# Kernel optimization log

Hardware: AMD Instinct MI355X
Metric: run time of the kernel (lower is better)

## Reference

```python
import jax, jax.numpy as jnp
import numpy as np

N_EMBD = 768
N_HEAD = 8
HEAD_DIM = N_EMBD // N_HEAD
EPS = 1e-5


def _layernorm(x, g, b):
    mu = jnp.mean(x, axis=-1, keepdims=True)
    var = jnp.mean(jnp.square(x - mu), axis=-1, keepdims=True)
    return (x - mu) * jax.lax.rsqrt(var + EPS) * g + b


def _new_gelu(x):
    c = jnp.sqrt(2.0 / jnp.pi).astype(x.dtype)
    return 0.5 * x * (1.0 + jnp.tanh(c * (x + 0.044715 * x * x * x)))


def setup_inputs() -> dict:
    key = jax.random.key(0)
    ks = jax.random.split(key, 10)
    B, T, C = 16, 1024, N_EMBD
    s = lambda fan_in: 1.0 / np.sqrt(fan_in)
    inp = {
        "x": jax.random.normal(ks[0], (B, T, C), dtype=jnp.float32),
        "ln1_g": jnp.ones((C,), jnp.float32),
        "ln1_b": jnp.zeros((C,), jnp.float32),
        "attn_w": jax.random.normal(ks[1], (C, 3 * C), jnp.float32) * s(C),
        "attn_b": jnp.zeros((3 * C,), jnp.float32),
        "proj_w": jax.random.normal(ks[2], (C, C), jnp.float32) * s(C),
        "proj_b": jnp.zeros((C,), jnp.float32),
        "ln2_g": jnp.ones((C,), jnp.float32),
        "ln2_b": jnp.zeros((C,), jnp.float32),
        "fc_w": jax.random.normal(ks[3], (C, 4 * C), jnp.float32) * s(C),
        "fc_b": jnp.zeros((4 * C,), jnp.float32),
        "fc2_w": jax.random.normal(ks[4], (4 * C, C), jnp.float32) * s(4 * C),
        "fc2_b": jnp.zeros((C,), jnp.float32),
    }
    return inp


def reference(x, ln1_g, ln1_b, attn_w, attn_b, proj_w, proj_b,
              ln2_g, ln2_b, fc_w, fc_b, fc2_w, fc2_b):
    B, T, C = x.shape
    H, D = N_HEAD, HEAD_DIM
    scale = 1.0 / np.sqrt(D)

    # --- attention branch ---
    h = _layernorm(x, ln1_g, ln1_b)
    qkv = h @ attn_w + attn_b                       # [B,T,3C]
    q, k, v = jnp.split(qkv, 3, axis=-1)
    q = q.reshape(B, T, H, D).transpose(0, 2, 1, 3)  # [B,H,T,D]
    k = k.reshape(B, T, H, D).transpose(0, 2, 1, 3)
    v = v.reshape(B, T, H, D).transpose(0, 2, 1, 3)
    att = jnp.einsum("bhqd,bhkd->bhqk", q, k) * scale
    causal = jnp.tril(jnp.ones((T, T), bool))
    att = jnp.where(causal, att, -jnp.inf)
    att = jax.nn.softmax(att, axis=-1)
    y = jnp.einsum("bhqk,bhkd->bhqd", att, v)        # [B,H,T,D]
    y = y.transpose(0, 2, 1, 3).reshape(B, T, C)
    y = y @ proj_w + proj_b
    x = x + y

    # --- MLP branch ---
    h2 = _layernorm(x, ln2_g, ln2_b)
    h2 = _new_gelu(h2 @ fc_w + fc_b)
    x = x + (h2 @ fc2_w + fc2_b)
    return x
```

## Files before the change

kernel.cpp:

```cpp
#include <hip/hip_runtime.h>


typedef __bf16 bf16;
typedef __bf16 bf16x8 __attribute__((ext_vector_type(8)));
typedef __bf16 bf16x4 __attribute__((ext_vector_type(4)));
typedef __bf16 bf16x2 __attribute__((ext_vector_type(2)));
typedef float f32x4 __attribute__((ext_vector_type(4)));

__device__ __forceinline__ void async_copy16(const void* g, void* l)
{
    __builtin_amdgcn_global_load_lds((__attribute__((address_space(1))) void*)g,
                                     (__attribute__((address_space(3))) void*)l,
                                     16, 0, 0);
}

__device__ __forceinline__ void bar_nodrain()
{
    __builtin_amdgcn_sched_barrier(0);
    __asm__ volatile("" ::: "memory");
    __builtin_amdgcn_s_barrier();
    __asm__ volatile("" ::: "memory");
    __builtin_amdgcn_sched_barrier(0);
}

__global__ __launch_bounds__(256) void wtrans4(const float* __restrict__ aw, bf16* __restrict__ awT,
                                               const float* __restrict__ pw, bf16* __restrict__ pwT,
                                               const float* __restrict__ fw, bf16* __restrict__ fwT,
                                               const float* __restrict__ f2w, bf16* __restrict__ f2wT)
{
    __shared__ float tile[32][33];
    int id = blockIdx.x;
    const float* in; bf16* out; int R, C, nx;
    if (id < 1728)      { in = aw;  out = awT;  R = 768;  C = 2304; nx = 72; }
    else if (id < 2304) { in = pw;  out = pwT;  R = 768;  C = 768;  nx = 24; id -= 1728; }
    else if (id < 4608) { in = fw;  out = fwT;  R = 768;  C = 3072; nx = 96; id -= 2304; }
    else                { in = f2w; out = f2wT; R = 3072; C = 768;  nx = 24; id -= 4608; }
    const int c0 = (id % nx) * 32, r0 = (id / nx) * 32;
    const int tx = threadIdx.x, ty = threadIdx.y;
#pragma unroll
    for (int i = 0; i < 4; ++i)
        tile[ty + i * 8][tx] = in[(size_t)(r0 + ty + i * 8) * C + c0 + tx];
    __syncthreads();
#pragma unroll
    for (int i = 0; i < 4; ++i)
        out[(size_t)(c0 + ty + i * 8) * R + r0 + tx] = (bf16)tile[tx][ty + i * 8];
}

template <typename TIN>
__global__ __launch_bounds__(256) void ln_kernel(const TIN* __restrict__ x,
                                                 const float* __restrict__ g,
                                                 const float* __restrict__ bb,
                                                 bf16* __restrict__ out)
{
    const int wave = threadIdx.x >> 6, lane = threadIdx.x & 63;
    const size_t row = (size_t)blockIdx.x * 4 + wave;
    const TIN* xr = x + row * 768;
    float v[12];
    float s = 0.f;
    if constexpr (sizeof(TIN) == 2) {
        const bf16x8 t8 = *(const bf16x8*)(xr + lane * 8);
        const bf16x4 t4 = *(const bf16x4*)(xr + 512 + lane * 4);
#pragma unroll
        for (int j = 0; j < 8; ++j) { v[j] = (float)t8[j]; s += v[j]; }
#pragma unroll
        for (int j = 0; j < 4; ++j) { v[8 + j] = (float)t4[j]; s += v[8 + j]; }
    } else {
#pragma unroll
        for (int c = 0; c < 3; ++c) {
            const float4 t4 = *(const float4*)(xr + c * 256 + lane * 4);
            v[c * 4 + 0] = t4.x; v[c * 4 + 1] = t4.y;
            v[c * 4 + 2] = t4.z; v[c * 4 + 3] = t4.w;
            s += t4.x + t4.y + t4.z + t4.w;
        }
    }
#pragma unroll
    for (int off = 32; off >= 1; off >>= 1) s += __shfl_xor(s, off, 64);
    const float mu = s * (1.f / 768.f);
    float q = 0.f;
#pragma unroll
    for (int i = 0; i < 12; ++i) { const float d = v[i] - mu; q += d * d; }
#pragma unroll
    for (int off = 32; off >= 1; off >>= 1) q += __shfl_xor(q, off, 64);
    const float rs = rsqrtf(q * (1.f / 768.f) + 1e-5f);

    if constexpr (sizeof(TIN) == 2) {
        bf16x8 o8; bf16x4 o4;
#pragma unroll
        for (int j = 0; j < 8; ++j) {
            const float gv = g[lane * 8 + j], bv = bb[lane * 8 + j];
            o8[j] = (bf16)((v[j] - mu) * rs * gv + bv);
        }
#pragma unroll
        for (int j = 0; j < 4; ++j) {
            const float gv = g[512 + lane * 4 + j], bv = bb[512 + lane * 4 + j];
            o4[j] = (bf16)((v[8 + j] - mu) * rs * gv + bv);
        }
        *(bf16x8*)(out + row * 768 + lane * 8) = o8;
        *(bf16x4*)(out + row * 768 + 512 + lane * 4) = o4;
    } else {
#pragma unroll
        for (int c = 0; c < 3; ++c) {
            const float4 gv = *(const float4*)(g + c * 256 + lane * 4);
            const float4 bv = *(const float4*)(bb + c * 256 + lane * 4);
            bf16x4 ov;
            ov[0] = (bf16)((v[c * 4 + 0] - mu) * rs * gv.x + bv.x);
            ov[1] = (bf16)((v[c * 4 + 1] - mu) * rs * gv.y + bv.y);
            ov[2] = (bf16)((v[c * 4 + 2] - mu) * rs * gv.z + bv.z);
            ov[3] = (bf16)((v[c * 4 + 3] - mu) * rs * gv.w + bv.w);
            *(bf16x4*)(out + row * 768 + c * 256 + lane * 4) = ov;
        }
    }
}

template <int EPI, int TN>
__global__ __launch_bounds__(256) void gemm_bt(const bf16* __restrict__ A,
                                               const bf16* __restrict__ Bt,
                                               const float* __restrict__ bias,
                                               const void* __restrict__ res,
                                               void* __restrict__ out,
                                               const int M, const int N, const int K)
{
    constexpr int NT_W = TN / 32;
    constexpr int NCPB = (TN * 8) / 256;
    __shared__ bf16 sA[2 * 128 * 32];
    __shared__ bf16 sB[2 * TN * 32];
    const int t = threadIdx.x;
    const int wave = t >> 6, lane = t & 63;
    const int quad = lane >> 4, l16 = lane & 15;
    const int bm0 = blockIdx.x * 128, bn0 = blockIdx.y * TN;
    const int wm = (wave >> 1) * 64, wn = (wave & 1) * (TN / 2);

    const f32x4 z4 = {0.f, 0.f, 0.f, 0.f};
    f32x4 acc[4][NT_W];
#pragma unroll
    for (int i = 0; i < 4; ++i)
#pragma unroll
        for (int j = 0; j < NT_W; ++j) acc[i][j] = z4;

    const bf16* gAp[4]; bf16* lAp[4];
#pragma unroll
    for (int c = 0; c < 4; ++c) {
        const int j = c * 256 + t;
        const int img = j >> 9, r = (j >> 2) & 127, k8 = j & 3;
        gAp[c] = A + (size_t)(bm0 + r) * K + img * 32 + k8 * 8;
        lAp[c] = sA + j * 8;
    }
    const bf16* gBp[NCPB]; bf16* lBp[NCPB];
#pragma unroll
    for (int c = 0; c < NCPB; ++c) {
        const int j = c * 256 + t;
        const int img = j / (TN * 4), r = (j % (TN * 4)) >> 2, k8 = j & 3;
        gBp[c] = Bt + (size_t)(bn0 + r) * K + img * 32 + k8 * 8;
        lBp[c] = sB + j * 8;
    }

    for (int kt = 0; kt < K; kt += 64) {
        __syncthreads();
#pragma unroll
        for (int c = 0; c < 4; ++c) async_copy16(gAp[c] + kt, lAp[c]);
#pragma unroll
        for (int c = 0; c < NCPB; ++c) async_copy16(gBp[c] + kt, lBp[c]);
        __syncthreads();

#pragma unroll
        for (int ks = 0; ks < 2; ++ks) {
            bf16x8 af[4], bfm[NT_W];
#pragma unroll
            for (int mt = 0; mt < 4; ++mt)
                af[mt] = *(const bf16x8*)(sA + ks * 4096 +
                                          (wm + mt * 16 + l16) * 32 + quad * 8);
#pragma unroll
            for (int nt = 0; nt < NT_W; ++nt)
                bfm[nt] = *(const bf16x8*)(sB + ks * (TN * 32) +
                                           (wn + nt * 16 + l16) * 32 + quad * 8);
#pragma unroll
            for (int mt = 0; mt < 4; ++mt)
#pragma unroll
                for (int nt = 0; nt < NT_W; ++nt)
                    acc[mt][nt] = __builtin_amdgcn_mfma_f32_16x16x32_bf16(
                        af[mt], bfm[nt], acc[mt][nt], 0, 0, 0);
        }
    }

    const int rb = bm0 + wm + quad * 4;
    const int cb = bn0 + wn + l16;
#pragma unroll
    for (int mt = 0; mt < 4; ++mt) {
#pragma unroll
        for (int nt = 0; nt < NT_W; ++nt) {
            const int col = cb + nt * 16;
            const float bv = bias[col];
#pragma unroll
            for (int reg = 0; reg < 4; ++reg) {
                const size_t idx = (size_t)(rb + mt * 16 + reg) * N + col;
                float v = acc[mt][nt][reg] + bv;
                if constexpr (EPI == 1) {
                    ((bf16*)out)[idx] = (bf16)(v + ((const float*)res)[idx]);
                } else if constexpr (EPI == 2) {
                    const float u = v;
                    const float a2 = 1.5957691216057308f *
                                     (u + 0.044715f * u * u * u);
                    v = u / (1.f + __expf(-a2));
                    ((bf16*)out)[idx] = (bf16)v;
                } else if constexpr (EPI == 3) {
                    ((float*)out)[idx] = v + (float)((const bf16*)res)[idx];
                } else {
                    ((bf16*)out)[idx] = (bf16)v;
                }
            }
        }
    }
}

__global__ __launch_bounds__(256) void attn_kernel(const bf16* __restrict__ qkv,
                                                   bf16* __restrict__ aout)
{
    constexpr int T = 1024, C3 = 2304, HD = 96, CC = 768;
    __shared__ bf16 sK[64 * 104];
    __shared__ bf16 sV[96 * 72];
    __shared__ bf16 sP[4][16 * 76];
    const int tid = threadIdx.x;
    const int wave = tid >> 6, lane = tid & 63;
    const int quad = lane >> 4, l16 = lane & 15;
    const int bh = blockIdx.x, b = bh >> 3, h = bh & 7;
    const float scale = 0.10206207261596575f;

    const int qAi = blockIdx.y;
    const int qBi = 15 - qAi;
    const int q0A = qAi * 64 + wave * 16;
    const int q0B = qBi * 64 + wave * 16;

    const bf16* kgbase = qkv + (size_t)b * T * C3 + CC + h * HD;
    const bf16* vgbase = qkv + (size_t)b * T * C3 + 2 * CC + h * HD;
    bf16* sPw = &sP[wave][0];

    int kKey[3], kCh[3], vKey2[3], vDq[3];
#pragma unroll
    for (int c = 0; c < 3; ++c) {
        const int j = c * 256 + tid;
        kKey[c] = j / 12; kCh[c] = j - kKey[c] * 12;
        vKey2[c] = (j & 31) * 2; vDq[c] = j >> 5;
    }

    const bf16* qrA = qkv + (size_t)(b * T + q0A + l16) * C3 + h * HD + quad * 8;
    const bf16* qrB = qkv + (size_t)(b * T + q0B + l16) * C3 + h * HD + quad * 8;
    const bf16x8 aQA0 = *(const bf16x8*)(qrA);
    const bf16x8 aQA1 = *(const bf16x8*)(qrA + 32);
    const bf16x8 aQA2 = *(const bf16x8*)(qrA + 64);
    const bf16x8 aQB0 = *(const bf16x8*)(qrB);
    const bf16x8 aQB1 = *(const bf16x8*)(qrB + 32);
    const bf16x8 aQB2 = *(const bf16x8*)(qrB + 64);

    const f32x4 z4 = {0.f, 0.f, 0.f, 0.f};
    f32x4 oA[6], oB[6];
#pragma unroll
    for (int i = 0; i < 6; ++i) { oA[i] = z4; oB[i] = z4; }
    float lA[4] = {0.f, 0.f, 0.f, 0.f}, lB[4] = {0.f, 0.f, 0.f, 0.f};

    bf16x8 kreg[3];
    bf16x4 va[3], vb[3];
    auto issue_tile = [&](const int kk0) {
#pragma unroll
        for (int c = 0; c < 3; ++c) {
            kreg[c] = *(const bf16x8*)(kgbase + (size_t)(kk0 + kKey[c]) * C3 +
                                       kCh[c] * 8);
            const bf16* p0 = vgbase + (size_t)(kk0 + vKey2[c]) * C3 + vDq[c] * 4;
            va[c] = *(const bf16x4*)p0;
            vb[c] = *(const bf16x4*)(p0 + C3);
        }
    };

    auto process = [&](const bf16x8& Q0, const bf16x8& Q1, const bf16x8& Q2,
                       f32x4 (&o)[6], float (&lrow)[4],
                       const int q0, const int kk0, const bool diag) {
        f32x4 s[4];
#pragma unroll
        for (int i = 0; i < 4; ++i) s[i] = z4;
#pragma unroll
        for (int nt = 0; nt < 4; ++nt) {
            const bf16* kp = sK + (nt * 16 + l16) * 104 + quad * 8;
            const bf16x8 b0 = *(const bf16x8*)(kp);
            const bf16x8 b1 = *(const bf16x8*)(kp + 32);
            const bf16x8 b2 = *(const bf16x8*)(kp + 64);
            s[nt] = __builtin_amdgcn_mfma_f32_16x16x32_bf16(Q0, b0, s[nt], 0, 0, 0);
            s[nt] = __builtin_amdgcn_mfma_f32_16x16x32_bf16(Q1, b1, s[nt], 0, 0, 0);
            s[nt] = __builtin_amdgcn_mfma_f32_16x16x32_bf16(Q2, b2, s[nt], 0, 0, 0);
        }

        float psum[4] = {0.f, 0.f, 0.f, 0.f};
#pragma unroll
        for (int nt = 0; nt < 4; ++nt)
#pragma unroll
            for (int reg = 0; reg < 4; ++reg) {
                float v = s[nt][reg] * scale;
                if (diag) {
                    const int qr = q0 + quad * 4 + reg;
                    const int key = kk0 + nt * 16 + l16;
                    v = (key > qr) ? -1e30f : v;
                }
                const float p = __expf(fminf(v, 30.f));
                s[nt][reg] = p;
                psum[reg] += p;
            }

#pragma unroll
        for (int nt = 0; nt < 4; ++nt)
#pragma unroll
            for (int reg = 0; reg < 4; ++reg)
                sPw[(quad * 4 + reg) * 76 + nt * 16 + l16] = (bf16)s[nt][reg];
        __asm__ volatile("s_waitcnt lgkmcnt(0)" ::: "memory");

#pragma unroll
        for (int off = 1; off < 16; off <<= 1)
#pragma unroll
            for (int reg = 0; reg < 4; ++reg)
                psum[reg] += __shfl_xor(psum[reg], off, 64);
#pragma unroll
        for (int reg = 0; reg < 4; ++reg) lrow[reg] += psum[reg];

        const bf16x8 aP0 = *(const bf16x8*)(sPw + l16 * 76 + quad * 8);
        const bf16x8 aP1 = *(const bf16x8*)(sPw + l16 * 76 + 32 + quad * 8);
#pragma unroll
        for (int dd = 0; dd < 6; ++dd) {
            const bf16* vp = sV + (dd * 16 + l16) * 72 + quad * 8;
            const bf16x8 v0 = *(const bf16x8*)(vp);
            const bf16x8 v1 = *(const bf16x8*)(vp + 32);
            o[dd] = __builtin_amdgcn_mfma_f32_16x16x32_bf16(aP0, v0, o[dd], 0, 0, 0);
            o[dd] = __builtin_amdgcn_mfma_f32_16x16x32_bf16(aP1, v1, o[dd], 0, 0, 0);
        }
    };

    issue_tile(0);

    for (int kb = 0; kb <= qBi; ++kb) {
        const int kk0 = kb * 64;

        bar_nodrain();

#pragma unroll
        for (int c = 0; c < 3; ++c)
            *(bf16x8*)(sK + kKey[c] * 104 + kCh[c] * 8) = kreg[c];
#pragma unroll
        for (int c = 0; c < 3; ++c) {
#pragma unroll
            for (int jj = 0; jj < 4; ++jj) {
                bf16x2 pk; pk[0] = va[c][jj]; pk[1] = vb[c][jj];
                *(bf16x2*)(sV + (vDq[c] * 4 + jj) * 72 + vKey2[c]) = pk;
            }
        }

        if (kb < qBi) issue_tile(kk0 + 64);

        __asm__ volatile("s_waitcnt lgkmcnt(0)" ::: "memory");
        bar_nodrain();

        process(aQB0, aQB1, aQB2, oB, lB, q0B, kk0, kb == qBi);
        if (kb <= qAi)
            process(aQA0, aQA1, aQA2, oA, lA, q0A, kk0, kb == qAi);
    }

    bf16* opA = aout + (size_t)(b * T + q0A + quad * 4) * CC + h * HD + l16;
    bf16* opB = aout + (size_t)(b * T + q0B + quad * 4) * CC + h * HD + l16;
#pragma unroll
    for (int reg = 0; reg < 4; ++reg) {
        const float invA = 1.f / lA[reg];
        const float invB = 1.f / lB[reg];
#pragma unroll
        for (int dd = 0; dd < 6; ++dd) {
            opA[(size_t)reg * CC + dd * 16] = (bf16)(oA[dd][reg] * invA);
            opB[(size_t)reg * CC + dd * 16] = (bf16)(oB[dd][reg] * invB);
        }
    }
}

extern "C" void kernel_launch(void* const* d_in, const int* in_sizes, int n_in,
                              void* d_out, int out_size, void* d_ws, size_t ws_size,
                              hipStream_t stream)
{
    const float* x      = (const float*)d_in[0];
    const float* ln1_g  = (const float*)d_in[1];
    const float* ln1_b  = (const float*)d_in[2];
    const float* attn_w = (const float*)d_in[3];
    const float* attn_b = (const float*)d_in[4];
    const float* proj_w = (const float*)d_in[5];
    const float* proj_b = (const float*)d_in[6];
    const float* ln2_g  = (const float*)d_in[7];
    const float* ln2_b  = (const float*)d_in[8];
    const float* fc_w   = (const float*)d_in[9];
    const float* fc_b   = (const float*)d_in[10];
    const float* fc2_w  = (const float*)d_in[11];
    const float* fc2_b  = (const float*)d_in[12];

    char* ws = (char*)d_ws;
    bf16*  attn_wT = (bf16*)(ws + 0);
    bf16*  proj_wT = (bf16*)(ws + 3538944);
    bf16*  fc_wT   = (bf16*)(ws + 4718592);
    bf16*  fc2_wT  = (bf16*)(ws + 9437184);
    bf16*  hbuf    = (bf16*)(ws + 14155776);
    bf16*  qkv     = (bf16*)(ws + 39321600);
    bf16*  x1      = (bf16*)(ws + 39321600);
    bf16*  act     = (bf16*)(ws + 64487424);

    wtrans4<<<6912, dim3(32, 8), 0, stream>>>(attn_w, attn_wT, proj_w, proj_wT,
                                              fc_w, fc_wT, fc2_w, fc2_wT);

    ln_kernel<float><<<4096, 256, 0, stream>>>(x, ln1_g, ln1_b, hbuf);

    gemm_bt<0, 128><<<dim3(128, 18), 256, 0, stream>>>(
        hbuf, attn_wT, attn_b, nullptr, qkv, 16384, 2304, 768);

    attn_kernel<<<dim3(128, 8), 256, 0, stream>>>(qkv, hbuf);

    gemm_bt<1, 128><<<dim3(128, 6), 256, 0, stream>>>(
        hbuf, proj_wT, proj_b, x, x1, 16384, 768, 768);

    ln_kernel<bf16><<<4096, 256, 0, stream>>>(x1, ln2_g, ln2_b, hbuf);

    for (int c = 0; c < 2; ++c) {
        const size_t ro = (size_t)c * 8192;
        gemm_bt<2, 128><<<dim3(64, 24), 256, 0, stream>>>(
            hbuf + ro * 768, fc_wT, fc_b, nullptr, act, 8192, 3072, 768);
        gemm_bt<3, 64><<<dim3(64, 12), 256, 0, stream>>>(
            act, fc2_wT, fc2_b, x1 + ro * 768,
            (float*)d_out + ro * 768, 8192, 768, 3072);
    }
}
```

Baseline: 596.4 us.

## Add 256x128-tile 512-thread GEMM kernel for QKV and FC projections

Adds a new GEMM kernel with 256x128 block tiles, 8 waves of 64x64 warp tiles, register-staged global-to-LDS double buffering and raised wave priority around the MFMA loop. It replaces the previous 128-row tiled gemm_bt for the QKV projection and the first MLP matmul (with its GELU epilogue). Larger tiles are meant to raise arithmetic intensity and cut global and LDS traffic per FLOP. The cost is more LDS per block, 512 threads and more accumulator registers, which lowers occupancy. It also halves the grid, so fewer blocks are available to fill the CUs.

Measured after the change: 598.3 us. No clear change (+0.3%).

```diff
diff --git a/kernel.cpp b/kernel.cpp
--- a/kernel.cpp
+++ b/kernel.cpp
@@ -212,6 +212,119 @@
     }
 }
 
+template <int EPI>
+__global__ __launch_bounds__(512) void gemm256(const bf16* __restrict__ A,
+                                               const bf16* __restrict__ Bt,
+                                               const float* __restrict__ bias,
+                                               bf16* __restrict__ out,
+                                               const int M, const int N, const int K)
+{
+    __shared__ bf16 sA[2][256 * 72];
+    __shared__ bf16 sB[2][128 * 72];
+    const int t = threadIdx.x;
+    const int wave = t >> 6, lane = t & 63;
+    const int quad = lane >> 4, l16 = lane & 15;
+    const int bm0 = blockIdx.x * 256, bn0 = blockIdx.y * 128;
+    const int wm = (wave >> 1) * 64, wn = (wave & 1) * 64;
+
+    const f32x4 z4 = {0.f, 0.f, 0.f, 0.f};
+    f32x4 acc[4][4];
+#pragma unroll
+    for (int i = 0; i < 4; ++i)
+#pragma unroll
+        for (int j = 0; j < 4; ++j) acc[i][j] = z4;
+
+    const bf16* gA[4]; int lA[4];
+#pragma unroll
+    for (int c = 0; c < 4; ++c) {
+        const int j = c * 512 + t, r = j >> 3, ch = j & 7;
+        gA[c] = A + (size_t)(bm0 + r) * K + ch * 8;
+        lA[c] = r * 72 + ch * 8;
+    }
+    const bf16* gB[2]; int lB[2];
+#pragma unroll
+    for (int c = 0; c < 2; ++c) {
+        const int j = c * 512 + t, r = j >> 3, ch = j & 7;
+        gB[c] = Bt + (size_t)(bn0 + r) * K + ch * 8;
+        lB[c] = r * 72 + ch * 8;
+    }
+
+    bf16x8 ra[4], rbv[2];
+    auto prefetch = [&](const int kt) {
+#pragma unroll
+        for (int c = 0; c < 4; ++c) ra[c] = *(const bf16x8*)(gA[c] + kt);
+#pragma unroll
+        for (int c = 0; c < 2; ++c) rbv[c] = *(const bf16x8*)(gB[c] + kt);
+    };
+    auto commit = [&](const int buf) {
+#pragma unroll
+        for (int c = 0; c < 4; ++c) *(bf16x8*)(&sA[buf][lA[c]]) = ra[c];
+#pragma unroll
+        for (int c = 0; c < 2; ++c) *(bf16x8*)(&sB[buf][lB[c]]) = rbv[c];
+    };
+
+    prefetch(0);
+    commit(0);
+    if (64 < K) prefetch(64);
+    __asm__ volatile("s_waitcnt lgkmcnt(0)" ::: "memory");
+    bar_nodrain();
+
+    int cur = 0;
+    for (int kt = 0; kt < K; kt += 64) {
+        if (kt + 64 < K) {
+            commit(cur ^ 1);
+            if (kt + 128 < K) prefetch(kt + 128);
+        }
+
+        __builtin_amdgcn_s_setprio(1);
+#pragma unroll
+        for (int ks = 0; ks < 2; ++ks) {
+            bf16x8 af[4], bfr[4];
+#pragma unroll
+            for (int mt = 0; mt < 4; ++mt)
+                af[mt] = *(const bf16x8*)(&sA[cur][(wm + mt * 16 + l16) * 72 +
+                                                   ks * 32 + quad * 8]);
+#pragma unroll
+            for (int nt = 0; nt < 4; ++nt)
+                bfr[nt] = *(const bf16x8*)(&sB[cur][(wn + nt * 16 + l16) * 72 +
+                                                    ks * 32 + quad * 8]);
+#pragma unroll
+            for (int mt = 0; mt < 4; ++mt)
+#pragma unroll
+                for (int nt = 0; nt < 4; ++nt)
+                    acc[mt][nt] = __builtin_amdgcn_mfma_f32_16x16x32_bf16(
+                        af[mt], bfr[nt], acc[mt][nt], 0, 0, 0);
+        }
+        __builtin_amdgcn_s_setprio(0);
+
+        __asm__ volatile("s_waitcnt lgkmcnt(0)" ::: "memory");
+        bar_nodrain();
+        cur ^= 1;
+    }
+
+    const int rb0 = bm0 + wm + quad * 4;
+    const int cb = bn0 + wn + l16;
+#pragma unroll
+    for (int mt = 0; mt < 4; ++mt) {
+#pragma unroll
+        for (int nt = 0; nt < 4; ++nt) {
+            const int col = cb + nt * 16;
+            const float bv = bias[col];
+#pragma unroll
+            for (int reg = 0; reg < 4; ++reg) {
+                const size_t idx = (size_t)(rb0 + mt * 16 + reg) * N + col;
+                float v = acc[mt][nt][reg] + bv;
+                if constexpr (EPI == 2) {
+                    const float a2 = 1.5957691216057308f *
+                                     (v + 0.044715f * v * v * v);
+                    v = v / (1.f + __expf(-a2));
+                }
+                out[idx] = (bf16)v;
+            }
+        }
+    }
+}
+
 __global__ __launch_bounds__(256) void attn_kernel(const bf16* __restrict__ qkv,
                                                    bf16* __restrict__ aout)
 {
@@ -406,8 +519,8 @@
 
     ln_kernel<float><<<4096, 256, 0, stream>>>(x, ln1_g, ln1_b, hbuf);
 
-    gemm_bt<0, 128><<<dim3(128, 18), 256, 0, stream>>>(
-        hbuf, attn_wT, attn_b, nullptr, qkv, 16384, 2304, 768);
+    gemm256<0><<<dim3(64, 18), 512, 0, stream>>>(
+        hbuf, attn_wT, attn_b, qkv, 16384, 2304, 768);
 
     attn_kernel<<<dim3(128, 8), 256, 0, stream>>>(qkv, hbuf);
 
@@ -418,8 +531,8 @@
 
     for (int c = 0; c < 2; ++c) {
         const size_t ro = (size_t)c * 8192;
-        gemm_bt<2, 128><<<dim3(64, 24), 256, 0, stream>>>(
-            hbuf + ro * 768, fc_wT, fc_b, nullptr, act, 8192, 3072, 768);
+        gemm256<2><<<dim3(32, 24), 512, 0, stream>>>(
+            hbuf + ro * 768, fc_wT, fc_b, act, 8192, 3072, 768);
         gemm_bt<3, 64><<<dim3(64, 12), 256, 0, stream>>>(
             act, fc2_wT, fc2_b, x1 + ro * 768,
             (float*)d_out + ro * 768, 8192, 768, 3072);
```
